# Optimization experiments

Hardware: AMD Instinct MI355X
Metric: run time of the kernel (lower is better)

Reference implementation:

```python
import jax, jax.numpy as jnp
import numpy as np

NDIM = 1024
NHEAD = 16
HEAD_DIM = NDIM // NHEAD


def setup_inputs() -> dict:
    key = jax.random.key(0)
    ks = jax.random.split(key, 12)
    B, L, C = 2, 2048, NDIM
    s = 0.02
    return {
        "q": jax.random.normal(ks[0], (B, L, C), jnp.float32),
        "k": jax.random.normal(ks[1], (B, L, C), jnp.float32),
        "v": jax.random.normal(ks[2], (B, L, C), jnp.float32),
        "Wq": jax.random.normal(ks[3], (C, C), jnp.float32) * s,
        "bq": jax.random.normal(ks[4], (C,), jnp.float32) * s,
        "Wk": jax.random.normal(ks[5], (C, C), jnp.float32) * s,
        "bk": jax.random.normal(ks[6], (C,), jnp.float32) * s,
        "Wv": jax.random.normal(ks[7], (C, C), jnp.float32) * s,
        "bv": jax.random.normal(ks[8], (C,), jnp.float32) * s,
        "Wo": jax.random.normal(ks[9], (C, C), jnp.float32) * s,
        "bo": jax.random.normal(ks[10], (C,), jnp.float32) * s,
    }


def reference(q, k, v, Wq, bq, Wk, bk, Wv, bv, Wo, bo):
    B, Lq, C = q.shape
    H, D = NHEAD, HEAD_DIM
    # projections, then split heads: (B, H, L, D)
    qh = (q @ Wq + bq).reshape(B, Lq, H, D).transpose(0, 2, 1, 3)
    kh = (k @ Wk + bk).reshape(B, k.shape[1], H, D).transpose(0, 2, 1, 3)
    vh = (v @ Wv + bv).reshape(B, v.shape[1], H, D).transpose(0, 2, 1, 3)
    scale = 1.0 / jnp.sqrt(jnp.asarray(D, qh.dtype))
    att = jnp.einsum("bhqd,bhkd->bhqk", qh, kh) * scale  # (B,H,Lq,Lk)
    att = jax.nn.softmax(att, axis=-1)  # dropout p=0.0 -> identity
    y = jnp.einsum("bhqk,bhkd->bhqd", att, vh)
    y = y.transpose(0, 2, 1, 3).reshape(B, Lq, C)
    return y @ Wo + bo
```

## Files before the change

### kernel.cpp

```cpp
#include <hip/hip_runtime.h>
#include <math.h>

#define BATCH 2
#define SEQ   2048
#define CDIM  1024
#define NHEAD 16
#define HDIM  64
#define TOKS  (BATCH * SEQ)

typedef __bf16 bf16x8 __attribute__((ext_vector_type(8)));
typedef __bf16 bf16x2 __attribute__((ext_vector_type(2)));
typedef float  f32x4  __attribute__((ext_vector_type(4)));

#define MFMA16(a, b, c) __builtin_amdgcn_mfma_f32_16x16x32_bf16(a, b, c, 0, 0, 0)

#define QSCALE 0.1803368801111204f

__device__ __forceinline__ void gload_lds16(const __bf16* g, __bf16* l) {
    __builtin_amdgcn_global_load_lds(
        (const __attribute__((address_space(1))) unsigned int*)g,
        (__attribute__((address_space(3))) unsigned int*)l, 16, 0, 0);
}

__global__ __launch_bounds__(256) void prep_kernel(
    const float* __restrict__ q, const float* __restrict__ k, const float* __restrict__ v,
    __bf16* __restrict__ qo, __bf16* __restrict__ ko, __bf16* __restrict__ vo,
    const float* __restrict__ W0, const float* __restrict__ W1,
    const float* __restrict__ W2, const float* __restrict__ W3,
    __bf16* __restrict__ T0, __bf16* __restrict__ T1,
    __bf16* __restrict__ T2, __bf16* __restrict__ T3)
{
    __shared__ __bf16 Ts[64][72];
    const int bx = blockIdx.x;
    const int tid = threadIdx.x;

    if (bx < 6144) {
        const int t = bx >> 11;
        const size_t i = ((size_t)(bx & 2047) * 256 + tid) * 8;
        const float* s = t == 0 ? q : (t == 1 ? k : v);
        __bf16* d = t == 0 ? qo : (t == 1 ? ko : vo);
        const float4 x = *(const float4*)&s[i];
        const float4 y = *(const float4*)&s[i + 4];
        bf16x8 o;
        o[0] = (__bf16)x.x; o[1] = (__bf16)x.y; o[2] = (__bf16)x.z; o[3] = (__bf16)x.w;
        o[4] = (__bf16)y.x; o[5] = (__bf16)y.y; o[6] = (__bf16)y.z; o[7] = (__bf16)y.w;
        *(bf16x8*)&d[i] = o;
        return;
    }

    const int t  = bx - 6144;
    const int z  = t >> 8;
    const int ry = (t & 255) >> 4;
    const int rx = t & 15;
    const float* W = z == 0 ? W0 : z == 1 ? W1 : z == 2 ? W2 : W3;
    __bf16* T = z == 0 ? T0 : z == 1 ? T1 : z == 2 ? T2 : T3;
    const int rb = ry * 64, cb = rx * 64;
    const int r = tid >> 4;
    const int c4 = (tid & 15) * 4;
#pragma unroll
    for (int p = 0; p < 4; p++) {
        const int rr = p * 16 + r;
        const float4 w4 = *(const float4*)&W[(size_t)(rb + rr) * CDIM + cb + c4];
        Ts[c4 + 0][rr] = (__bf16)w4.x;
        Ts[c4 + 1][rr] = (__bf16)w4.y;
        Ts[c4 + 2][rr] = (__bf16)w4.z;
        Ts[c4 + 3][rr] = (__bf16)w4.w;
    }
    __syncthreads();
    const int n = tid >> 2;
    const int k16 = (tid & 3) * 16;
    *(bf16x8*)&T[(size_t)(cb + n) * CDIM + rb + k16]     = *(const bf16x8*)&Ts[n][k16];
    *(bf16x8*)&T[(size_t)(cb + n) * CDIM + rb + k16 + 8] = *(const bf16x8*)&Ts[n][k16 + 8];
}

__global__ __launch_bounds__(512, 6) void qkv_gemm_kernel(
    const __bf16* __restrict__ qb, const __bf16* __restrict__ kb,
    const __bf16* __restrict__ vb,
    const __bf16* __restrict__ Wqt, const __bf16* __restrict__ Wkt,
    const __bf16* __restrict__ Wvt,
    const float* __restrict__ bq, const float* __restrict__ bk,
    const float* __restrict__ bv,
    __bf16* __restrict__ Qh, __bf16* __restrict__ Kh, __bf16* __restrict__ Vht)
{
    __shared__ __bf16 As[128 * 32];
    __shared__ __bf16 Bs[128 * 32];

    const int lin = blockIdx.x + (blockIdx.y << 3) + (blockIdx.z << 8);
    const int nl  = (lin & 7) * 96 + (lin >> 3);
    const int bx  = nl & 7;
    const int by  = (nl >> 3) & 31;
    const int z   = nl >> 8;

    const __bf16* A    = z == 0 ? qb : z == 1 ? kb : Wvt;
    const __bf16* Bt   = z == 0 ? Wqt : z == 1 ? Wkt : vb;
    const float*  bias = z == 0 ? bq : z == 1 ? bk : bv;

    const int tid  = threadIdx.x;
    const int w    = tid >> 6;
    const int lane = tid & 63;
    const int quad = lane >> 4;
    const int c    = lane & 15;
    const int wm   = w >> 1;
    const int wn   = w & 1;
    const int rowBase = (z == 2 ? bx : by) * 128;
    const int colBase = (z == 2 ? by : bx) * 128;

    const int sr = lane >> 2;
    const int sk = (lane & 3) * 8;

    f32x4 acc[2][4];
#pragma unroll
    for (int i = 0; i < 2; i++)
#pragma unroll
        for (int j = 0; j < 4; j++) acc[i][j] = (f32x4){0, 0, 0, 0};

    const __bf16* srcA = A  + (size_t)(rowBase + w * 16 + sr) * CDIM + sk;
    const __bf16* srcB = Bt + (size_t)(colBase + w * 16 + sr) * CDIM + sk;
    __bf16* dstA = &As[w * 16 * 32];
    __bf16* dstB = &Bs[w * 16 * 32];

    for (int k0 = 0; k0 < CDIM; k0 += 32) {
        gload_lds16(srcA + k0, dstA);
        gload_lds16(srcB + k0, dstB);
        __syncthreads();

        bf16x8 af[2], bf[4];
#pragma unroll
        for (int i = 0; i < 2; i++)
            af[i] = *(const bf16x8*)&As[(wm * 32 + i * 16 + c) * 32 + quad * 8];
#pragma unroll
        for (int i = 0; i < 4; i++)
            bf[i] = *(const bf16x8*)&Bs[(wn * 64 + i * 16 + c) * 32 + quad * 8];
#pragma unroll
        for (int mi = 0; mi < 2; mi++)
#pragma unroll
            for (int ni = 0; ni < 4; ni++)
                acc[mi][ni] = MFMA16(af[mi], bf[ni], acc[mi][ni]);
        __syncthreads();
    }

#pragma unroll
    for (int mi = 0; mi < 2; mi++) {
#pragma unroll
        for (int ni = 0; ni < 4; ni++) {
            const int col = colBase + wn * 64 + ni * 16 + c;
#pragma unroll
            for (int r = 0; r < 4; r++) {
                const int row = rowBase + wm * 32 + mi * 16 + quad * 4 + r;
                const float val = acc[mi][ni][r];
                if (z == 2) {
                    const int col2 = (col & ~31) | (((col & 15) << 1) | ((col >> 4) & 1));
                    Vht[(size_t)row * TOKS + col2] = (__bf16)(val + bias[row]);
                } else {
                    const int b = row >> 11, l = row & 2047;
                    const int h = col >> 6,  d = col & 63;
                    const float s = (z == 0) ? QSCALE : 1.0f;
                    __bf16* outp = (z == 0) ? Qh : Kh;
                    outp[((((size_t)b * NHEAD + h) * SEQ) + l) * HDIM + d] =
                        (__bf16)((val + bias[col]) * s);
                }
            }
        }
    }
}

__global__ __launch_bounds__(512, 4) void out_gemm_kernel(
    const __bf16* __restrict__ A, const __bf16* __restrict__ Bt,
    const float* __restrict__ bias, float* __restrict__ out)
{
    __shared__ __bf16 As[128 * 32];
    __shared__ __bf16 Bs[64 * 32];

    const int lin = blockIdx.x + (blockIdx.y << 4);
    const int nl  = (lin & 7) * 64 + (lin >> 3);
    const int bx  = nl & 15;
    const int by  = nl >> 4;

    const int tid  = threadIdx.x;
    const int w    = tid >> 6;
    const int lane = tid & 63;
    const int quad = lane >> 4;
    const int c    = lane & 15;
    const int wm   = w >> 1;
    const int wn   = w & 1;
    const int rowBase = by * 128;
    const int colBase = bx * 64;
    const int sr = lane >> 2;
    const int sk = (lane & 3) * 8;

    f32x4 acc[2][2];
#pragma unroll
    for (int i = 0; i < 2; i++)
#pragma unroll
        for (int j = 0; j < 2; j++) acc[i][j] = (f32x4){0, 0, 0, 0};

    const __bf16* srcA = A + (size_t)(rowBase + w * 16 + sr) * CDIM + sk;
    const __bf16* srcB = Bt + (size_t)(colBase + (w & 3) * 16 + sr) * CDIM + sk;
    __bf16* dstA = &As[w * 16 * 32];
    __bf16* dstB = &Bs[(w & 3) * 16 * 32];

    for (int k0 = 0; k0 < CDIM; k0 += 32) {
        gload_lds16(srcA + k0, dstA);
        if (w < 4) gload_lds16(srcB + k0, dstB);
        __syncthreads();

        bf16x8 af[2], bf[2];
#pragma unroll
        for (int i = 0; i < 2; i++)
            af[i] = *(const bf16x8*)&As[(wm * 32 + i * 16 + c) * 32 + quad * 8];
#pragma unroll
        for (int i = 0; i < 2; i++)
            bf[i] = *(const bf16x8*)&Bs[(wn * 32 + i * 16 + c) * 32 + quad * 8];
#pragma unroll
        for (int mi = 0; mi < 2; mi++)
#pragma unroll
            for (int ni = 0; ni < 2; ni++)
                acc[mi][ni] = MFMA16(af[mi], bf[ni], acc[mi][ni]);
        __syncthreads();
    }

#pragma unroll
    for (int mi = 0; mi < 2; mi++) {
#pragma unroll
        for (int ni = 0; ni < 2; ni++) {
            const int col = colBase + wn * 32 + ni * 16 + c;
#pragma unroll
            for (int r = 0; r < 4; r++) {
                const int row = rowBase + wm * 32 + mi * 16 + quad * 4 + r;
                out[(size_t)row * CDIM + col] = acc[mi][ni][r] + bias[col];
            }
        }
    }
}

__global__ __launch_bounds__(512, 4) void attn_v6_kernel(
    const __bf16* __restrict__ Qh, const __bf16* __restrict__ Kh,
    const __bf16* __restrict__ Vht, __bf16* __restrict__ Y)
{
    __shared__ __align__(16) __bf16 Ks[2][64][72];
    __shared__ __align__(16) __bf16 Vt[2][64][72];
    __shared__ __align__(16) unsigned int Pf[8][16][36];

    const int tid  = threadIdx.x;
    const int w    = tid >> 6;
    const int lane = tid & 63;
    const int quad = lane >> 4;
    const int c    = lane & 15;
    const int bh   = blockIdx.x;
    const int b    = bh >> 4;
    const int h    = bh & 15;
    const int qbase = blockIdx.y * 128 + w * 16;

    const __bf16* Qg = Qh + (size_t)bh * SEQ * HDIM;
    const __bf16* Kg = Kh + (size_t)bh * SEQ * HDIM;
    const __bf16* Vg = Vht + (size_t)(h * HDIM) * TOKS + (size_t)b * SEQ;

    bf16x8 qf[2];
    qf[0] = *(const bf16x8*)&Qg[(size_t)(qbase + c) * HDIM + quad * 8];
    qf[1] = *(const bf16x8*)&Qg[(size_t)(qbase + c) * HDIM + 32 + quad * 8];

    bf16x8 ones;
#pragma unroll
    for (int j = 0; j < 8; j++) ones[j] = (__bf16)1.0f;

    f32x4 O[4];
    f32x4 L = (f32x4){0, 0, 0, 0};
#pragma unroll
    for (int i = 0; i < 4; i++) O[i] = (f32x4){0, 0, 0, 0};

    const int srow = tid >> 3;
    const int scol = (tid & 7) * 8;

    *(bf16x8*)&Ks[0][srow][scol] = *(const bf16x8*)&Kg[(size_t)srow * HDIM + scol];
    *(bf16x8*)&Vt[0][srow][scol] = *(const bf16x8*)&Vg[(size_t)srow * TOKS + scol];
    __syncthreads();

    int buf = 0;
    for (int t0 = 0; t0 < SEQ; t0 += 64) {
        const int tn = t0 + 64;
        bf16x8 kpre, vpre;
        if (tn < SEQ) {
            kpre = *(const bf16x8*)&Kg[(size_t)(tn + srow) * HDIM + scol];
            vpre = *(const bf16x8*)&Vg[(size_t)srow * TOKS + tn + scol];
        }

        f32x4 s[4];
#pragma unroll
        for (int j = 0; j < 4; j++) {
            const bf16x8 k0 = *(const bf16x8*)&Ks[buf][j * 16 + c][quad * 8];
            const bf16x8 k1 = *(const bf16x8*)&Ks[buf][j * 16 + c][32 + quad * 8];
            f32x4 t = {0, 0, 0, 0};
            t = MFMA16(qf[0], k0, t);
            t = MFMA16(qf[1], k1, t);
            s[j] = t;
        }

#pragma unroll
        for (int r = 0; r < 4; r++) {
            union { bf16x2 v; unsigned int u; } pa, pb;
            pa.v[0] = (__bf16)__builtin_amdgcn_exp2f(s[0][r]);
            pa.v[1] = (__bf16)__builtin_amdgcn_exp2f(s[1][r]);
            pb.v[0] = (__bf16)__builtin_amdgcn_exp2f(s[2][r]);
            pb.v[1] = (__bf16)__builtin_amdgcn_exp2f(s[3][r]);
            Pf[w][quad * 4 + r][c]      = pa.u;
            Pf[w][quad * 4 + r][16 + c] = pb.u;
        }
        const bf16x8 pf0 = *(const bf16x8*)&Pf[w][c][quad * 4];
        const bf16x8 pf1 = *(const bf16x8*)&Pf[w][c][16 + quad * 4];

        __builtin_amdgcn_s_setprio(1);
        L = MFMA16(pf0, ones, L);
        L = MFMA16(pf1, ones, L);
#pragma unroll
        for (int i = 0; i < 4; i++) {
            const bf16x8 vA = *(const bf16x8*)&Vt[buf][16 * i + c][quad * 8];
            const bf16x8 vB = *(const bf16x8*)&Vt[buf][16 * i + c][32 + quad * 8];
            O[i] = MFMA16(pf0, vA, O[i]);
            O[i] = MFMA16(pf1, vB, O[i]);
        }
        __builtin_amdgcn_s_setprio(0);

        if (tn < SEQ) {
            *(bf16x8*)&Ks[buf ^ 1][srow][scol] = kpre;
            *(bf16x8*)&Vt[buf ^ 1][srow][scol] = vpre;
        }
        __syncthreads();
        buf ^= 1;
    }

    __bf16* Yb = Y + (size_t)b * SEQ * CDIM;
#pragma unroll
    for (int r = 0; r < 4; r++) {
        const float inv = 1.0f / L[r];
        const int l = qbase + quad * 4 + r;
        __bf16* yp = Yb + (size_t)l * CDIM + h * HDIM + c;
        yp[0]  = (__bf16)(O[0][r] * inv);
        yp[16] = (__bf16)(O[1][r] * inv);
        yp[32] = (__bf16)(O[2][r] * inv);
        yp[48] = (__bf16)(O[3][r] * inv);
    }
}


extern "C" void kernel_launch(void* const* d_in, const int* in_sizes, int n_in,
                              void* d_out, int out_size, void* d_ws, size_t ws_size,
                              hipStream_t stream)
{
    const float* q  = (const float*)d_in[0];
    const float* k  = (const float*)d_in[1];
    const float* v  = (const float*)d_in[2];
    const float* Wq = (const float*)d_in[3];
    const float* bq = (const float*)d_in[4];
    const float* Wk = (const float*)d_in[5];
    const float* bk = (const float*)d_in[6];
    const float* Wv = (const float*)d_in[7];
    const float* bv = (const float*)d_in[8];
    const float* Wo = (const float*)d_in[9];
    const float* bo = (const float*)d_in[10];
    float* out = (float*)d_out;

    const size_t MAT = (size_t)TOKS * CDIM;
    const size_t WN  = (size_t)CDIM * CDIM;

    __bf16* p   = (__bf16*)d_ws;
    __bf16* qb  = p; p += MAT;
    __bf16* kb  = p; p += MAT;
    __bf16* vb  = p; p += MAT;
    __bf16* Wqt = p; p += WN;
    __bf16* Wkt = p; p += WN;
    __bf16* Wvt = p; p += WN;
    __bf16* Wot = p; p += WN;
    __bf16* Qh  = p; p += MAT;
    __bf16* Kh  = p; p += MAT;
    __bf16* Vht = p; p += MAT;
    __bf16* Yb  = qb;

    prep_kernel<<<dim3(7168), dim3(256), 0, stream>>>(
        q, k, v, qb, kb, vb, Wq, Wk, Wv, Wo, Wqt, Wkt, Wvt, Wot);

    qkv_gemm_kernel<<<dim3(8, 32, 3), dim3(512), 0, stream>>>(
        qb, kb, vb, Wqt, Wkt, Wvt, bq, bk, bv, Qh, Kh, Vht);

    attn_v6_kernel<<<dim3(BATCH * NHEAD, SEQ / 128), dim3(512), 0, stream>>>(Qh, Kh, Vht, Yb);

    out_gemm_kernel<<<dim3(16, 32), dim3(512), 0, stream>>>(Yb, Wot, bo, out);
}
```

Before: 225.5 us.

## Rewrite attention with 32x32 MFMA and register-resident probabilities

```diff
diff --git a/kernel.cpp b/kernel.cpp
--- a/kernel.cpp
+++ b/kernel.cpp
@@ -11,8 +11,10 @@
 typedef __bf16 bf16x8 __attribute__((ext_vector_type(8)));
 typedef __bf16 bf16x2 __attribute__((ext_vector_type(2)));
 typedef float  f32x4  __attribute__((ext_vector_type(4)));
+typedef float  f32x16 __attribute__((ext_vector_type(16)));
 
 #define MFMA16(a, b, c) __builtin_amdgcn_mfma_f32_16x16x32_bf16(a, b, c, 0, 0, 0)
+#define MFMA32(a, b, c) __builtin_amdgcn_mfma_f32_32x32x16_bf16(a, b, c, 0, 0, 0)
 
 #define QSCALE 0.1803368801111204f
 
@@ -149,8 +151,7 @@
                 const int row = rowBase + wm * 32 + mi * 16 + quad * 4 + r;
                 const float val = acc[mi][ni][r];
                 if (z == 2) {
-                    const int col2 = (col & ~31) | (((col & 15) << 1) | ((col >> 4) & 1));
-                    Vht[(size_t)row * TOKS + col2] = (__bf16)(val + bias[row]);
+                    Vht[(size_t)row * TOKS + col] = (__bf16)(val + bias[row]);
                 } else {
                     const int b = row >> 11, l = row & 2047;
                     const int h = col >> 6,  d = col & 63;
@@ -233,111 +234,129 @@
     }
 }
 
-__global__ __launch_bounds__(512, 4) void attn_v6_kernel(
+__global__ __launch_bounds__(256, 2) void attn_v7_kernel(
     const __bf16* __restrict__ Qh, const __bf16* __restrict__ Kh,
     const __bf16* __restrict__ Vht, __bf16* __restrict__ Y)
 {
     __shared__ __align__(16) __bf16 Ks[2][64][72];
     __shared__ __align__(16) __bf16 Vt[2][64][72];
-    __shared__ __align__(16) unsigned int Pf[8][16][36];
 
     const int tid  = threadIdx.x;
     const int w    = tid >> 6;
     const int lane = tid & 63;
-    const int quad = lane >> 4;
-    const int c    = lane & 15;
+    const int l31  = lane & 31;
+    const int hi   = lane >> 5;
     const int bh   = blockIdx.x;
     const int b    = bh >> 4;
     const int h    = bh & 15;
-    const int qbase = blockIdx.y * 128 + w * 16;
+    const int qbase = blockIdx.y * 128 + w * 32;
 
     const __bf16* Qg = Qh + (size_t)bh * SEQ * HDIM;
     const __bf16* Kg = Kh + (size_t)bh * SEQ * HDIM;
     const __bf16* Vg = Vht + (size_t)(h * HDIM) * TOKS + (size_t)b * SEQ;
 
-    bf16x8 qf[2];
-    qf[0] = *(const bf16x8*)&Qg[(size_t)(qbase + c) * HDIM + quad * 8];
-    qf[1] = *(const bf16x8*)&Qg[(size_t)(qbase + c) * HDIM + 32 + quad * 8];
-
-    bf16x8 ones;
-#pragma unroll
-    for (int j = 0; j < 8; j++) ones[j] = (__bf16)1.0f;
-
-    f32x4 O[4];
-    f32x4 L = (f32x4){0, 0, 0, 0};
-#pragma unroll
-    for (int i = 0; i < 4; i++) O[i] = (f32x4){0, 0, 0, 0};
-
-    const int srow = tid >> 3;
-    const int scol = (tid & 7) * 8;
-
-    *(bf16x8*)&Ks[0][srow][scol] = *(const bf16x8*)&Kg[(size_t)srow * HDIM + scol];
-    *(bf16x8*)&Vt[0][srow][scol] = *(const bf16x8*)&Vg[(size_t)srow * TOKS + scol];
+    bf16x8 qf[4];
+#pragma unroll
+    for (int ks = 0; ks < 4; ks++)
+        qf[ks] = *(const bf16x8*)&Qg[(size_t)(qbase + l31) * HDIM + ks * 16 + hi * 8];
+
+    f32x16 O[2];
+#pragma unroll
+    for (int i = 0; i < 2; i++)
+#pragma unroll
+        for (int j = 0; j < 16; j++) O[i][j] = 0.0f;
+    float Lp = 0.0f;
+
+    const int srow = tid >> 2;
+    const int scol = (tid & 3) * 16;
+
+    *(bf16x8*)&Ks[0][srow][scol]     = *(const bf16x8*)&Kg[(size_t)srow * HDIM + scol];
+    *(bf16x8*)&Ks[0][srow][scol + 8] = *(const bf16x8*)&Kg[(size_t)srow * HDIM + scol + 8];
+    *(bf16x8*)&Vt[0][srow][scol]     = *(const bf16x8*)&Vg[(size_t)srow * TOKS + scol];
+    *(bf16x8*)&Vt[0][srow][scol + 8] = *(const bf16x8*)&Vg[(size_t)srow * TOKS + scol + 8];
     __syncthreads();
 
     int buf = 0;
     for (int t0 = 0; t0 < SEQ; t0 += 64) {
         const int tn = t0 + 64;
-        bf16x8 kpre, vpre;
+        bf16x8 kp0, kp1, vp0, vp1;
         if (tn < SEQ) {
-            kpre = *(const bf16x8*)&Kg[(size_t)(tn + srow) * HDIM + scol];
-            vpre = *(const bf16x8*)&Vg[(size_t)srow * TOKS + tn + scol];
+            kp0 = *(const bf16x8*)&Kg[(size_t)(tn + srow) * HDIM + scol];
+            kp1 = *(const bf16x8*)&Kg[(size_t)(tn + srow) * HDIM + scol + 8];
+            vp0 = *(const bf16x8*)&Vg[(size_t)srow * TOKS + tn + scol];
+            vp1 = *(const bf16x8*)&Vg[(size_t)srow * TOKS + tn + scol + 8];
         }
 
-        f32x4 s[4];
-#pragma unroll
-        for (int j = 0; j < 4; j++) {
-            const bf16x8 k0 = *(const bf16x8*)&Ks[buf][j * 16 + c][quad * 8];
-            const bf16x8 k1 = *(const bf16x8*)&Ks[buf][j * 16 + c][32 + quad * 8];
-            f32x4 t = {0, 0, 0, 0};
-            t = MFMA16(qf[0], k0, t);
-            t = MFMA16(qf[1], k1, t);
-            s[j] = t;
+#pragma unroll
+        for (int kt = 0; kt < 2; kt++) {
+            f32x16 st;
+#pragma unroll
+            for (int j = 0; j < 16; j++) st[j] = 0.0f;
+            __builtin_amdgcn_s_setprio(1);
+#pragma unroll
+            for (int ks = 0; ks < 4; ks++) {
+                const bf16x8 kf =
+                    *(const bf16x8*)&Ks[buf][kt * 32 + l31][ks * 16 + hi * 8];
+                st = MFMA32(kf, qf[ks], st);
+            }
+            __builtin_amdgcn_s_setprio(0);
+
+            float p[16];
+#pragma unroll
+            for (int j = 0; j < 16; j++) p[j] = __builtin_amdgcn_exp2f(st[j]);
+
+#pragma unroll
+            for (int kl = 0; kl < 2; kl++) {
+                const int r0 = kl * 8;
+                union { bf16x2 v; unsigned int u; } pa, pb, pc, pd;
+                pa.v[0] = (__bf16)p[r0 + 0]; pa.v[1] = (__bf16)p[r0 + 1];
+                pb.v[0] = (__bf16)p[r0 + 2]; pb.v[1] = (__bf16)p[r0 + 3];
+                pc.v[0] = (__bf16)p[r0 + 4]; pc.v[1] = (__bf16)p[r0 + 5];
+                pd.v[0] = (__bf16)p[r0 + 6]; pd.v[1] = (__bf16)p[r0 + 7];
+                Lp += (float)pa.v[0] + (float)pa.v[1] + (float)pb.v[0] + (float)pb.v[1]
+                    + (float)pc.v[0] + (float)pc.v[1] + (float)pd.v[0] + (float)pd.v[1];
+                const unsigned int ax = __shfl_xor(pa.u, 32);
+                const unsigned int bx = __shfl_xor(pb.u, 32);
+                const unsigned int cx = __shfl_xor(pc.u, 32);
+                const unsigned int dx = __shfl_xor(pd.u, 32);
+                union { unsigned int u[4]; bf16x8 v; } af;
+                af.u[0] = hi ? cx : pa.u;
+                af.u[1] = hi ? dx : pb.u;
+                af.u[2] = hi ? pc.u : ax;
+                af.u[3] = hi ? pd.u : bx;
+                const int kcol = kt * 32 + kl * 16 + hi * 8;
+                __builtin_amdgcn_s_setprio(1);
+#pragma unroll
+                for (int dt = 0; dt < 2; dt++) {
+                    const bf16x8 vf =
+                        *(const bf16x8*)&Vt[buf][dt * 32 + l31][kcol];
+                    O[dt] = MFMA32(af.v, vf, O[dt]);
+                }
+                __builtin_amdgcn_s_setprio(0);
+            }
         }
 
-#pragma unroll
-        for (int r = 0; r < 4; r++) {
-            union { bf16x2 v; unsigned int u; } pa, pb;
-            pa.v[0] = (__bf16)__builtin_amdgcn_exp2f(s[0][r]);
-            pa.v[1] = (__bf16)__builtin_amdgcn_exp2f(s[1][r]);
-            pb.v[0] = (__bf16)__builtin_amdgcn_exp2f(s[2][r]);
-            pb.v[1] = (__bf16)__builtin_amdgcn_exp2f(s[3][r]);
-            Pf[w][quad * 4 + r][c]      = pa.u;
-            Pf[w][quad * 4 + r][16 + c] = pb.u;
-        }
-        const bf16x8 pf0 = *(const bf16x8*)&Pf[w][c][quad * 4];
-        const bf16x8 pf1 = *(const bf16x8*)&Pf[w][c][16 + quad * 4];
-
-        __builtin_amdgcn_s_setprio(1);
-        L = MFMA16(pf0, ones, L);
-        L = MFMA16(pf1, ones, L);
-#pragma unroll
-        for (int i = 0; i < 4; i++) {
-            const bf16x8 vA = *(const bf16x8*)&Vt[buf][16 * i + c][quad * 8];
-            const bf16x8 vB = *(const bf16x8*)&Vt[buf][16 * i + c][32 + quad * 8];
-            O[i] = MFMA16(pf0, vA, O[i]);
-            O[i] = MFMA16(pf1, vB, O[i]);
-        }
-        __builtin_amdgcn_s_setprio(0);
-
         if (tn < SEQ) {
-            *(bf16x8*)&Ks[buf ^ 1][srow][scol] = kpre;
-            *(bf16x8*)&Vt[buf ^ 1][srow][scol] = vpre;
+            *(bf16x8*)&Ks[buf ^ 1][srow][scol]     = kp0;
+            *(bf16x8*)&Ks[buf ^ 1][srow][scol + 8] = kp1;
+            *(bf16x8*)&Vt[buf ^ 1][srow][scol]     = vp0;
+            *(bf16x8*)&Vt[buf ^ 1][srow][scol + 8] = vp1;
         }
         __syncthreads();
         buf ^= 1;
     }
 
+    const float Lt  = Lp + __shfl_xor(Lp, 32);
+    const float inv = 1.0f / Lt;
+
     __bf16* Yb = Y + (size_t)b * SEQ * CDIM;
 #pragma unroll
-    for (int r = 0; r < 4; r++) {
-        const float inv = 1.0f / L[r];
-        const int l = qbase + quad * 4 + r;
-        __bf16* yp = Yb + (size_t)l * CDIM + h * HDIM + c;
-        yp[0]  = (__bf16)(O[0][r] * inv);
-        yp[16] = (__bf16)(O[1][r] * inv);
-        yp[32] = (__bf16)(O[2][r] * inv);
-        yp[48] = (__bf16)(O[3][r] * inv);
+    for (int reg = 0; reg < 16; reg++) {
+        const int qrow  = (reg & 3) + 8 * (reg >> 2) + 4 * hi;
+        const float iq  = __shfl(inv, qrow);
+        __bf16* yp = Yb + (size_t)(qbase + qrow) * CDIM + h * HDIM + l31;
+        yp[0]  = (__bf16)(O[0][reg] * iq);
+        yp[32] = (__bf16)(O[1][reg] * iq);
     }
 }
 
@@ -381,7 +400,7 @@
     qkv_gemm_kernel<<<dim3(8, 32, 3), dim3(512), 0, stream>>>(
         qb, kb, vb, Wqt, Wkt, Wvt, bq, bk, bv, Qh, Kh, Vht);
 
-    attn_v6_kernel<<<dim3(BATCH * NHEAD, SEQ / 128), dim3(512), 0, stream>>>(Qh, Kh, Vht, Yb);
+    attn_v7_kernel<<<dim3(BATCH * NHEAD, SEQ / 128), dim3(256), 0, stream>>>(Qh, Kh, Vht, Yb);
 
     out_gemm_kernel<<<dim3(16, 32), dim3(512), 0, stream>>>(Yb, Wot, bo, out);
 }
```

Result: no change. 227.2 us (+0.8%).
